# Performance work log

Hardware: AMD Instinct MI355X
Metric: run time of the kernel (lower is better)

Reference implementation:

```python
import jax, jax.numpy as jnp
import numpy as np

T, B, D, H = 512, 256, 64, 128  # timesteps, num_envs, obs_dim, lstm hidden


def setup_inputs() -> dict:
    key = jax.random.key(0)
    ks = jax.random.split(key, 8)
    x = jax.random.normal(ks[0], (T, B, D), dtype=jnp.float32)
    done = (jax.random.uniform(ks[1], (T, B)) < 0.02).astype(jnp.float32)
    h0 = 0.01 * jax.random.normal(ks[2], (B, H), dtype=jnp.float32)
    c0 = 0.01 * jax.random.normal(ks[3], (B, H), dtype=jnp.float32)
    W_ih = jax.random.normal(ks[4], (4 * H, D), dtype=jnp.float32) / np.sqrt(D)
    W_hh = jax.random.normal(ks[5], (4 * H, H), dtype=jnp.float32) / np.sqrt(H)
    b_ih = jnp.zeros((4 * H,), dtype=jnp.float32)
    b_hh = jnp.zeros((4 * H,), dtype=jnp.float32)
    W_hid = jax.random.normal(ks[6], (H, H), dtype=jnp.float32) * np.sqrt(2.0 / H)
    b_hid = jnp.zeros((H,), dtype=jnp.float32)
    return {"x": x, "done": done, "h0": h0, "c0": c0,
            "W_ih": W_ih, "b_ih": b_ih, "W_hh": W_hh, "b_hh": b_hh,
            "W_hid": W_hid, "b_hid": b_hid}


def reference(x, done, h0, c0, W_ih, b_ih, W_hh, b_hh, W_hid, b_hid):
    # Precompute input contribution to gates for all timesteps: [T, B, 4H]
    xg = jnp.einsum('tbd,gd->tbg', x, W_ih) + b_ih + b_hh

    def step(carry, inp):
        h, c = carry            # [B, H] each
        xg_t, d = inp           # [B, 4H], [B]
        mask = (1.0 - d)[:, None]
        h = h * mask            # reset state where episode ended
        c = c * mask
        gates = xg_t + h @ W_hh.T            # [B, 4H]
        i, f, g, o = jnp.split(gates, 4, axis=-1)  # PyTorch gate order i,f,g,o
        c = jax.nn.sigmoid(f) * c + jax.nn.sigmoid(i) * jnp.tanh(g)
        h = jax.nn.sigmoid(o) * jnp.tanh(c)
        return (h, c), h

    (_, _), hs = jax.lax.scan(step, (h0, c0), (xg, done))  # hs: [T, B, H]
    hidden = hs.reshape(-1, H) @ W_hid.T + b_hid           # [T*B, H]
    return hidden
```

## Files before the change

### kernel.cpp

```cpp
#include <hip/hip_runtime.h>

#define T_STEPS 512
#define B_ENV   256
#define D_IN    64
#define H_DIM   128
#define G4      512

typedef _Float16 h2v __attribute__((ext_vector_type(2)));
typedef _Float16 h8v __attribute__((ext_vector_type(8)));
typedef float    f4v __attribute__((ext_vector_type(4)));
typedef __fp16   g2  __attribute__((ext_vector_type(2)));
typedef __fp16   g8  __attribute__((ext_vector_type(8)));

__device__ __forceinline__ float dot2(h2v a, h2v b, float c) {
#if __has_builtin(__builtin_amdgcn_fdot2)
    return __builtin_amdgcn_fdot2(a, b, c, false);
#else
    return c + (float)a.x * (float)b.x + (float)a.y * (float)b.y;
#endif
}

__device__ __forceinline__ g2 pack16g(float a, float b) {
#if __has_builtin(__builtin_amdgcn_cvt_pkrtz)
    return __builtin_amdgcn_cvt_pkrtz(a, b);
#else
    g2 p; p.x = (__fp16)a; p.y = (__fp16)b; return p;
#endif
}
__device__ __forceinline__ h2v pack16(float a, float b) {
    union { g2 r; h2v h; } u; u.r = pack16g(a, b); return u.h;
}

__device__ __forceinline__ f4v mfma16(g8 a, g8 b, f4v c) {
    return __builtin_amdgcn_mfma_f32_16x16x32_f16(a, b, c, 0, 0, 0);
}

__device__ __forceinline__ float fast_rcp(float x) {
#if __has_builtin(__builtin_amdgcn_rcpf)
    return __builtin_amdgcn_rcpf(x);
#else
    return 1.0f / x;
#endif
}
__device__ __forceinline__ float sigm(float x)   { return fast_rcp(1.0f + __expf(-x)); }
__device__ __forceinline__ float tanh_f(float x) { float e = __expf(2.0f * x); return 1.0f - 2.0f * fast_rcp(e + 1.0f); }

template <int CTRL>
__device__ __forceinline__ float dpp_mov(float v) {
    int s = __builtin_amdgcn_update_dpp(
        0, __builtin_bit_cast(int, v), CTRL, 0xF, 0xF, true);
    return __builtin_bit_cast(float, s);
}
__device__ __forceinline__ float quad_allreduce(float v) {
    v += dpp_mov<0xB1>(v);
    v += dpp_mov<0x4E>(v);
    return v;
}

__device__ __forceinline__ void sync_lds() {
    asm volatile("s_waitcnt lgkmcnt(0)" ::: "memory");
    __builtin_amdgcn_s_barrier();
    asm volatile("" ::: "memory");
}

__global__ __launch_bounds__(256)
void ppo_xg(const float* __restrict__ x,
            const float* __restrict__ W_ih,
            unsigned short* __restrict__ xg)
{
    const int tid  = threadIdx.x;
    const int lane = tid & 63;
    const int w    = tid >> 6;
    const int rml  = lane & 15;
    const int colg = lane >> 4;

    __shared__ h2v wl[G4][36];

    #pragma unroll
    for (int i = 0; i < 32; ++i) {
        const int idx = tid + 256 * i;
        const int r = idx >> 4, cc = idx & 15;
        f4v v = *reinterpret_cast<const f4v*>(W_ih + (size_t)idx * 4);
        wl[r][2 * cc]     = pack16(v.x, v.y);
        wl[r][2 * cc + 1] = pack16(v.z, v.w);
    }
    __syncthreads();

    const size_t row0 = (size_t)blockIdx.x * 64 + w * 16;

    g8 a[2];
    #pragma unroll
    for (int ks = 0; ks < 2; ++ks) {
        const float* p = x + (row0 + rml) * D_IN + ks * 32 + colg * 8;
        union { g2 q[4]; g8 v; } u;
        #pragma unroll
        for (int c = 0; c < 4; ++c) u.q[c] = pack16g(p[2 * c], p[2 * c + 1]);
        a[ks] = u.v;
    }

    #pragma unroll 4
    for (int ct = 0; ct < 32; ++ct) {
        const int col = ct * 16 + rml;
        const g8 b0 = *reinterpret_cast<const g8*>(&wl[col][colg * 4]);
        const g8 b1 = *reinterpret_cast<const g8*>(&wl[col][16 + colg * 4]);
        f4v acc = {0.f, 0.f, 0.f, 0.f};
        acc = mfma16(a[0], b0, acc);
        acc = mfma16(a[1], b1, acc);
        #pragma unroll
        for (int reg = 0; reg < 4; ++reg) {
            const __fp16 hv = (__fp16)acc[reg];
            xg[(row0 + colg * 4 + reg) * G4 + ct * 16 + rml] =
                __builtin_bit_cast(unsigned short, hv);
        }
    }
}

__global__ __launch_bounds__(512, 1) __attribute__((amdgpu_waves_per_eu(2, 2)))
void ppo_lstm_scan_xg(const unsigned short* __restrict__ xg,
                      const float* __restrict__ done,
                      const float* __restrict__ h0,
                      const float* __restrict__ c0,
                      const float* __restrict__ b_ih,
                      const float* __restrict__ W_hh,
                      const float* __restrict__ b_hh,
                      float* __restrict__ hs)
{
    const int b   = blockIdx.x;
    const int tid = threadIdx.x;
    const int qq  = tid & 3;
    const int j   = tid >> 2;

    __shared__ alignas(16) h2v   h16[2][H_DIM / 2];
    __shared__ alignas(16) float smask[T_STEPS];

    h2v whh[64];
    #pragma unroll
    for (int g = 0; g < 4; ++g) {
        const float* wr = W_hh + (size_t)(g * H_DIM + j) * H_DIM + qq * 32;
        #pragma unroll
        for (int c = 0; c < 16; ++c)
            whh[g * 16 + c] = pack16(wr[2 * c], wr[2 * c + 1]);
    }
    const int   r_own    = qq * H_DIM + j;
    const float bias_own = b_ih[r_own] + b_hh[r_own];
    float       c_reg    = c0[b * H_DIM + j];

    smask[tid] = 1.0f - done[(size_t)tid * B_ENV + b];
    if (tid < 64) {
        const float sm0 = 1.0f - done[b];
        const float* hp = h0 + b * H_DIM;
        h16[0][tid] = pack16(hp[2 * tid] * sm0, hp[2 * tid + 1] * sm0);
    }
    const unsigned short* xgp = xg + (size_t)b * G4 + r_own;
    unsigned short xcur = xgp[0];
    __syncthreads();

    float dm = 1.0f - done[b];

    for (int t = 0; t < T_STEPS; ++t) {
        const int rb = t & 1, wb = rb ^ 1;

        const int tn = (t + 1 < T_STEPS) ? (t + 1) : t;
        const unsigned short xnext = xgp[(size_t)tn * B_ENV * G4];

        const h8v* hp8 = reinterpret_cast<const h8v*>(&h16[rb][qq * 16]);
        float s0 = 0.f, s1 = 0.f, s2 = 0.f, s3 = 0.f;
        #pragma unroll
        for (int c4 = 0; c4 < 4; ++c4) {
            union { h8v v; h2v p[4]; } u;
            u.v = hp8[c4];
            #pragma unroll
            for (int pp = 0; pp < 4; ++pp) {
                s0 = dot2(whh[      c4 * 4 + pp], u.p[pp], s0);
                s1 = dot2(whh[16 +  c4 * 4 + pp], u.p[pp], s1);
                s2 = dot2(whh[32 +  c4 * 4 + pp], u.p[pp], s2);
                s3 = dot2(whh[48 +  c4 * 4 + pp], u.p[pp], s3);
            }
        }

        s0 = quad_allreduce(s0);
        s1 = quad_allreduce(s1);
        s2 = quad_allreduce(s2);
        s3 = quad_allreduce(s3);

        const float xgf = (float)__builtin_bit_cast(__fp16, xcur);
        const float s01 = (qq & 1) ? s1 : s0;
        const float s23 = (qq & 1) ? s3 : s2;
        const float gs  = ((qq & 2) ? s23 : s01) + bias_own + xgf;
        const float av  = (qq == 2) ? tanh_f(gs) : sigm(gs);
        const float ai  = dpp_mov<0x00>(av);
        const float af  = dpp_mov<0x55>(av);
        const float ag  = dpp_mov<0xAA>(av);
        const float ao  = dpp_mov<0xFF>(av);

        const float cn = af * (c_reg * dm) + ai * ag;
        c_reg = cn;
        const float hn = ao * tanh_f(cn);

        const float smn = smask[(t + 1 < T_STEPS) ? (t + 1) : (T_STEPS - 1)];
        if (qq == 0) {
            reinterpret_cast<_Float16*>(h16[wb])[j] = (_Float16)(hn * smn);
            hs[((size_t)t * B_ENV + b) * H_DIM + j] = hn;
        }
        dm   = smn;
        xcur = xnext;
        sync_lds();
    }
}

__global__ __launch_bounds__(512, 1) __attribute__((amdgpu_waves_per_eu(2, 2)))
void ppo_lstm_scan_fb(const float* __restrict__ x,
                      const float* __restrict__ done,
                      const float* __restrict__ h0,
                      const float* __restrict__ c0,
                      const float* __restrict__ W_ih,
                      const float* __restrict__ b_ih,
                      const float* __restrict__ W_hh,
                      const float* __restrict__ b_hh,
                      float* __restrict__ hs)
{
    const int b   = blockIdx.x;
    const int tid = threadIdx.x;
    const int qq  = tid & 3;
    const int j   = tid >> 2;

    __shared__ alignas(16) h2v   h16[2][H_DIM / 2];
    __shared__ alignas(16) float smask[T_STEPS];

    h2v whh[64];
    h2v wih[32];
    #pragma unroll
    for (int g = 0; g < 4; ++g) {
        const float* wr = W_hh + (size_t)(g * H_DIM + j) * H_DIM + qq * 32;
        #pragma unroll
        for (int c = 0; c < 16; ++c)
            whh[g * 16 + c] = pack16(wr[2 * c], wr[2 * c + 1]);
        const float* wr2 = W_ih + (size_t)(g * H_DIM + j) * D_IN + qq * 16;
        #pragma unroll
        for (int c = 0; c < 8; ++c)
            wih[g * 8 + c] = pack16(wr2[2 * c], wr2[2 * c + 1]);
    }
    const int   r_own    = qq * H_DIM + j;
    const float bias_own = b_ih[r_own] + b_hh[r_own];
    float       c_reg    = c0[b * H_DIM + j];

    smask[tid] = 1.0f - done[(size_t)tid * B_ENV + b];
    if (tid < 64) {
        const float sm0 = 1.0f - done[b];
        const float* hp = h0 + b * H_DIM;
        h16[0][tid] = pack16(hp[2 * tid] * sm0, hp[2 * tid + 1] * sm0);
    }
    f4v xr[4];
    {
        const float* xp = x + (size_t)b * D_IN + qq * 16;
        #pragma unroll
        for (int i = 0; i < 4; ++i)
            xr[i] = *reinterpret_cast<const f4v*>(xp + 4 * i);
    }
    __syncthreads();

    for (int t = 0; t < T_STEPS; ++t) {
        const int rb = t & 1, wb = rb ^ 1;

        h2v xh[8];
        #pragma unroll
        for (int i = 0; i < 4; ++i) {
            xh[2 * i]     = pack16(xr[i].x, xr[i].y);
            xh[2 * i + 1] = pack16(xr[i].z, xr[i].w);
        }
        {
            const int tn = (t + 1 < T_STEPS) ? (t + 1) : t;
            const float* xp = x + ((size_t)tn * B_ENV + b) * D_IN + qq * 16;
            #pragma unroll
            for (int i = 0; i < 4; ++i)
                xr[i] = *reinterpret_cast<const f4v*>(xp + 4 * i);
        }

        const h8v* hp8 = reinterpret_cast<const h8v*>(&h16[rb][qq * 16]);
        float s0 = 0.f, s1 = 0.f, s2 = 0.f, s3 = 0.f;
        #pragma unroll
        for (int c4 = 0; c4 < 4; ++c4) {
            union { h8v v; h2v p[4]; } u;
            u.v = hp8[c4];
            #pragma unroll
            for (int pp = 0; pp < 4; ++pp) {
                s0 = dot2(whh[      c4 * 4 + pp], u.p[pp], s0);
                s1 = dot2(whh[16 +  c4 * 4 + pp], u.p[pp], s1);
                s2 = dot2(whh[32 +  c4 * 4 + pp], u.p[pp], s2);
                s3 = dot2(whh[48 +  c4 * 4 + pp], u.p[pp], s3);
            }
        }
        #pragma unroll
        for (int c = 0; c < 8; ++c) {
            s0 = dot2(wih[     c], xh[c], s0);
            s1 = dot2(wih[ 8 + c], xh[c], s1);
            s2 = dot2(wih[16 + c], xh[c], s2);
            s3 = dot2(wih[24 + c], xh[c], s3);
        }

        s0 = quad_allreduce(s0);
        s1 = quad_allreduce(s1);
        s2 = quad_allreduce(s2);
        s3 = quad_allreduce(s3);

        const float s01 = (qq & 1) ? s1 : s0;
        const float s23 = (qq & 1) ? s3 : s2;
        const float gs  = ((qq & 2) ? s23 : s01) + bias_own;
        const float av  = (qq == 2) ? tanh_f(gs) : sigm(gs);
        const float ai  = dpp_mov<0x00>(av);
        const float af  = dpp_mov<0x55>(av);
        const float ag  = dpp_mov<0xAA>(av);
        const float ao  = dpp_mov<0xFF>(av);

        const float dm = smask[t];
        const float cn = af * (c_reg * dm) + ai * ag;
        c_reg = cn;
        const float hn = ao * tanh_f(cn);

        if (qq == 0) {
            const float smn = smask[(t + 1 < T_STEPS) ? (t + 1) : (T_STEPS - 1)];
            reinterpret_cast<_Float16*>(h16[wb])[j] = (_Float16)(hn * smn);
            hs[((size_t)t * B_ENV + b) * H_DIM + j] = hn;
        }
        sync_lds();
    }
}

#define PADK 68
__global__ __launch_bounds__(256)
void ppo_proj(const float* __restrict__ W_hid,
              const float* __restrict__ b_hid,
              float* __restrict__ out)
{
    __shared__ h2v wl[H_DIM][PADK];
    __shared__ h2v hl[H_DIM][PADK];
    const int tid = threadIdx.x;
    const int rg  = tid >> 4;
    const int cg  = tid & 15;

    const size_t r0 = (size_t)blockIdx.x * H_DIM;

    #pragma unroll
    for (int i = 0; i < 16; ++i) {
        const int idx = tid + 256 * i;
        const int r = idx >> 5, cc = idx & 31;
        f4v v = *reinterpret_cast<const f4v*>(W_hid + 4 * (size_t)idx);
        wl[r][2 * cc]     = pack16(v.x, v.y);
        wl[r][2 * cc + 1] = pack16(v.z, v.w);
    }
    #pragma unroll
    for (int i = 0; i < 16; ++i) {
        const int idx = tid + 256 * i;
        const int r = idx >> 5, cc = idx & 31;
        f4v v = *reinterpret_cast<const f4v*>(out + (r0 + r) * H_DIM + 4 * cc);
        hl[r][2 * cc]     = pack16(v.x, v.y);
        hl[r][2 * cc + 1] = pack16(v.z, v.w);
    }
    float bcol[8];
    #pragma unroll
    for (int jj = 0; jj < 8; ++jj) bcol[jj] = b_hid[cg + 16 * jj];
    __syncthreads();

    float acc[8][8];
    #pragma unroll
    for (int i = 0; i < 8; ++i)
        #pragma unroll
        for (int jj = 0; jj < 8; ++jj) acc[i][jj] = 0.f;

    for (int kq = 0; kq < 16; ++kq) {
        union { h8v v; h2v p[4]; } hv[8], wv[8];
        #pragma unroll
        for (int i = 0; i < 8; ++i)
            hv[i].v = *reinterpret_cast<const h8v*>(&hl[rg * 8 + i][4 * kq]);
        #pragma unroll
        for (int jj = 0; jj < 8; ++jj)
            wv[jj].v = *reinterpret_cast<const h8v*>(&wl[cg + 16 * jj][4 * kq]);
        #pragma unroll
        for (int i = 0; i < 8; ++i)
            #pragma unroll
            for (int jj = 0; jj < 8; ++jj) {
                acc[i][jj] = dot2(hv[i].p[0], wv[jj].p[0], acc[i][jj]);
                acc[i][jj] = dot2(hv[i].p[1], wv[jj].p[1], acc[i][jj]);
                acc[i][jj] = dot2(hv[i].p[2], wv[jj].p[2], acc[i][jj]);
                acc[i][jj] = dot2(hv[i].p[3], wv[jj].p[3], acc[i][jj]);
            }
    }

    #pragma unroll
    for (int i = 0; i < 8; ++i)
        #pragma unroll
        for (int jj = 0; jj < 8; ++jj)
            out[(r0 + rg * 8 + i) * H_DIM + cg + 16 * jj] = acc[i][jj] + bcol[jj];
}

extern "C" void kernel_launch(void* const* d_in, const int* in_sizes, int n_in,
                              void* d_out, int out_size, void* d_ws, size_t ws_size,
                              hipStream_t stream) {
    const float* x     = (const float*)d_in[0];
    const float* done  = (const float*)d_in[1];
    const float* h0    = (const float*)d_in[2];
    const float* c0    = (const float*)d_in[3];
    const float* W_ih  = (const float*)d_in[4];
    const float* b_ih  = (const float*)d_in[5];
    const float* W_hh  = (const float*)d_in[6];
    const float* b_hh  = (const float*)d_in[7];
    const float* W_hid = (const float*)d_in[8];
    const float* b_hid = (const float*)d_in[9];
    float* out = (float*)d_out;
    (void)n_in; (void)in_sizes; (void)out_size;

    const size_t xg_bytes = (size_t)T_STEPS * B_ENV * G4 * sizeof(unsigned short);
    if (ws_size >= xg_bytes) {
        unsigned short* xg = (unsigned short*)d_ws;
        hipLaunchKernelGGL(ppo_xg, dim3((T_STEPS * B_ENV) / 64), dim3(256), 0, stream,
                           x, W_ih, xg);
        hipLaunchKernelGGL(ppo_lstm_scan_xg, dim3(B_ENV), dim3(512), 0, stream,
                           xg, done, h0, c0, b_ih, W_hh, b_hh, out);
    } else {
        hipLaunchKernelGGL(ppo_lstm_scan_fb, dim3(B_ENV), dim3(512), 0, stream,
                           x, done, h0, c0, W_ih, b_ih, W_hh, b_hh, out);
    }
    hipLaunchKernelGGL(ppo_proj, dim3((T_STEPS * B_ENV) / H_DIM), dim3(256), 0, stream,
                       W_hid, b_hid, out);
}
```

Before: 367.7 us.

## Compute all four LSTM gates redundantly per lane and fold bias into xg

The per-step gate path is restructured. Each lane's xg value is injected into the partial sums with one-hot masks before the quad all-reduce. Every lane then evaluates all four gate activations itself, which removes the per-lane gate select and the four DPP broadcasts from the serial critical path. The bias add moves into the xg precompute kernel's MFMA accumulator initialisation. The loop now uses pointer increments, unroll 2 and a peeled last step so the per-step boundary clamps go away. The trade-off is four transcendental activations per lane instead of one, which raises ALU work on each timestep.

Result: slower. 399.9 us (+8.7%).

```diff
diff --git a/kernel.cpp b/kernel.cpp
--- a/kernel.cpp
+++ b/kernel.cpp
@@ -66,6 +66,8 @@
 __global__ __launch_bounds__(256)
 void ppo_xg(const float* __restrict__ x,
             const float* __restrict__ W_ih,
+            const float* __restrict__ b_ih,
+            const float* __restrict__ b_hh,
             unsigned short* __restrict__ xg)
 {
     const int tid  = threadIdx.x;
@@ -74,7 +76,8 @@
     const int rml  = lane & 15;
     const int colg = lane >> 4;
 
-    __shared__ h2v wl[G4][36];
+    __shared__ h2v   wl[G4][36];
+    __shared__ float bl[G4];
 
     #pragma unroll
     for (int i = 0; i < 32; ++i) {
@@ -84,6 +87,8 @@
         wl[r][2 * cc]     = pack16(v.x, v.y);
         wl[r][2 * cc + 1] = pack16(v.z, v.w);
     }
+    bl[tid]       = b_ih[tid]       + b_hh[tid];
+    bl[tid + 256] = b_ih[tid + 256] + b_hh[tid + 256];
     __syncthreads();
 
     const size_t row0 = (size_t)blockIdx.x * 64 + w * 16;
@@ -103,7 +108,8 @@
         const int col = ct * 16 + rml;
         const g8 b0 = *reinterpret_cast<const g8*>(&wl[col][colg * 4]);
         const g8 b1 = *reinterpret_cast<const g8*>(&wl[col][16 + colg * 4]);
-        f4v acc = {0.f, 0.f, 0.f, 0.f};
+        const float bb = bl[col];
+        f4v acc = {bb, bb, bb, bb};
         acc = mfma16(a[0], b0, acc);
         acc = mfma16(a[1], b1, acc);
         #pragma unroll
@@ -120,9 +126,7 @@
                       const float* __restrict__ done,
                       const float* __restrict__ h0,
                       const float* __restrict__ c0,
-                      const float* __restrict__ b_ih,
                       const float* __restrict__ W_hh,
-                      const float* __restrict__ b_hh,
                       float* __restrict__ hs)
 {
     const int b   = blockIdx.x;
@@ -141,9 +145,11 @@
         for (int c = 0; c < 16; ++c)
             whh[g * 16 + c] = pack16(wr[2 * c], wr[2 * c + 1]);
     }
-    const int   r_own    = qq * H_DIM + j;
-    const float bias_own = b_ih[r_own] + b_hh[r_own];
-    float       c_reg    = c0[b * H_DIM + j];
+    const float m0 = (qq == 0) ? 1.f : 0.f;
+    const float m1 = (qq == 1) ? 1.f : 0.f;
+    const float m2 = (qq == 2) ? 1.f : 0.f;
+    const float m3 = (qq == 3) ? 1.f : 0.f;
+    float c_reg = c0[b * H_DIM + j];
 
     smask[tid] = 1.0f - done[(size_t)tid * B_ENV + b];
     if (tid < 64) {
@@ -151,20 +157,25 @@
         const float* hp = h0 + b * H_DIM;
         h16[0][tid] = pack16(hp[2 * tid] * sm0, hp[2 * tid + 1] * sm0);
     }
-    const unsigned short* xgp = xg + (size_t)b * G4 + r_own;
+    const size_t XSTR = (size_t)B_ENV * G4;
+    const unsigned short* xgp = xg + (size_t)b * G4 + (qq * H_DIM + j);
     unsigned short xcur = xgp[0];
+    float* hsp = hs + (size_t)b * H_DIM + j;
     __syncthreads();
 
     float dm = 1.0f - done[b];
 
-    for (int t = 0; t < T_STEPS; ++t) {
+    #pragma unroll 2
+    for (int t = 0; t < T_STEPS - 1; ++t) {
         const int rb = t & 1, wb = rb ^ 1;
 
-        const int tn = (t + 1 < T_STEPS) ? (t + 1) : t;
-        const unsigned short xnext = xgp[(size_t)tn * B_ENV * G4];
+        const float xgf = (float)__builtin_bit_cast(__fp16, xcur);
+        float s0 = xgf * m0, s1 = xgf * m1, s2 = xgf * m2, s3 = xgf * m3;
+
+        xgp += XSTR;
+        const unsigned short xnext = xgp[0];
 
         const h8v* hp8 = reinterpret_cast<const h8v*>(&h16[rb][qq * 16]);
-        float s0 = 0.f, s1 = 0.f, s2 = 0.f, s3 = 0.f;
         #pragma unroll
         for (int c4 = 0; c4 < 4; ++c4) {
             union { h8v v; h2v p[4]; } u;
@@ -183,28 +194,54 @@
         s2 = quad_allreduce(s2);
         s3 = quad_allreduce(s3);
 
-        const float xgf = (float)__builtin_bit_cast(__fp16, xcur);
-        const float s01 = (qq & 1) ? s1 : s0;
-        const float s23 = (qq & 1) ? s3 : s2;
-        const float gs  = ((qq & 2) ? s23 : s01) + bias_own + xgf;
-        const float av  = (qq == 2) ? tanh_f(gs) : sigm(gs);
-        const float ai  = dpp_mov<0x00>(av);
-        const float af  = dpp_mov<0x55>(av);
-        const float ag  = dpp_mov<0xAA>(av);
-        const float ao  = dpp_mov<0xFF>(av);
-
-        const float cn = af * (c_reg * dm) + ai * ag;
+        const float gi = sigm(s0);
+        const float gf = sigm(s1);
+        const float gg = tanh_f(s2);
+        const float go = sigm(s3);
+
+        const float cn = gf * (c_reg * dm) + gi * gg;
         c_reg = cn;
-        const float hn = ao * tanh_f(cn);
-
-        const float smn = smask[(t + 1 < T_STEPS) ? (t + 1) : (T_STEPS - 1)];
+        const float hn = go * tanh_f(cn);
+
+        const float smn = smask[t + 1];
         if (qq == 0) {
             reinterpret_cast<_Float16*>(h16[wb])[j] = (_Float16)(hn * smn);
-            hs[((size_t)t * B_ENV + b) * H_DIM + j] = hn;
-        }
+            hsp[0] = hn;
+        }
+        hsp += (size_t)B_ENV * H_DIM;
         dm   = smn;
         xcur = xnext;
         sync_lds();
+    }
+
+    {
+        const int rb = (T_STEPS - 1) & 1;
+        const float xgf = (float)__builtin_bit_cast(__fp16, xcur);
+        float s0 = xgf * m0, s1 = xgf * m1, s2 = xgf * m2, s3 = xgf * m3;
+        const h8v* hp8 = reinterpret_cast<const h8v*>(&h16[rb][qq * 16]);
+        #pragma unroll
+        for (int c4 = 0; c4 < 4; ++c4) {
+            union { h8v v; h2v p[4]; } u;
+            u.v = hp8[c4];
+            #pragma unroll
+            for (int pp = 0; pp < 4; ++pp) {
+                s0 = dot2(whh[      c4 * 4 + pp], u.p[pp], s0);
+                s1 = dot2(whh[16 +  c4 * 4 + pp], u.p[pp], s1);
+                s2 = dot2(whh[32 +  c4 * 4 + pp], u.p[pp], s2);
+                s3 = dot2(whh[48 +  c4 * 4 + pp], u.p[pp], s3);
+            }
+        }
+        s0 = quad_allreduce(s0);
+        s1 = quad_allreduce(s1);
+        s2 = quad_allreduce(s2);
+        s3 = quad_allreduce(s3);
+        const float gi = sigm(s0);
+        const float gf = sigm(s1);
+        const float gg = tanh_f(s2);
+        const float go = sigm(s3);
+        const float cn = gf * (c_reg * dm) + gi * gg;
+        const float hn = go * tanh_f(cn);
+        if (qq == 0) hsp[0] = hn;
     }
 }
 
@@ -413,9 +450,9 @@
     if (ws_size >= xg_bytes) {
         unsigned short* xg = (unsigned short*)d_ws;
         hipLaunchKernelGGL(ppo_xg, dim3((T_STEPS * B_ENV) / 64), dim3(256), 0, stream,
-                           x, W_ih, xg);
+                           x, W_ih, b_ih, b_hh, xg);
         hipLaunchKernelGGL(ppo_lstm_scan_xg, dim3(B_ENV), dim3(512), 0, stream,
-                           xg, done, h0, c0, b_ih, W_hh, b_hh, out);
+                           xg, done, h0, c0, W_hh, out);
     } else {
         hipLaunchKernelGGL(ppo_lstm_scan_fb, dim3(B_ENV), dim3(512), 0, stream,
                            x, done, h0, c0, W_ih, b_ih, W_hh, b_hh, out);
```
